# Kernel tuning notes

Hardware: AMD Instinct MI355X
Metric: run time of the kernel (lower is better)

Reference implementation:

```python
import jax, jax.numpy as jnp
import numpy as np


def mha(x, mask, wq, bq, wk, bk, wv, bv, wo, bo, n_heads):
    # Flaubert/XLM MultiHeadAttention (eval mode, dropout = identity).
    bs, qlen, dim = x.shape
    dph = dim // n_heads

    def split_heads(t):  # (bs, qlen, dim) -> (bs, n_heads, qlen, dph)
        return t.reshape(bs, qlen, n_heads, dph).transpose(0, 2, 1, 3)

    q = split_heads(x @ wq + bq) / jnp.sqrt(jnp.asarray(dph, x.dtype))
    k = split_heads(x @ wk + bk)
    v = split_heads(x @ wv + bv)

    scores = jnp.einsum('bhqd,bhkd->bhqk', q, k)  # (bs, h, qlen, klen)
    neg = jnp.finfo(scores.dtype).min
    scores = jnp.where((mask == 0)[:, None, None, :], neg, scores)
    weights = jax.nn.softmax(scores, axis=-1)
    ctx = jnp.einsum('bhqk,bhkd->bhqd', weights, v)
    ctx = ctx.transpose(0, 2, 1, 3).reshape(bs, qlen, dim)
    return ctx @ wo + bo


def setup_inputs() -> dict:
    key = jax.random.key(0)
    ks = jax.random.split(key, 20)
    bs, slen = 4, 1024
    d0, d1 = 192, 66
    std = 0.02
    inp = {
        'x': jax.random.normal(ks[0], (bs, slen, d0), jnp.float32),
        'y': jax.random.normal(ks[1], (bs, slen, d1), jnp.float32),
        'mask0': jax.random.randint(ks[2], (bs, slen), 0, 2, jnp.int32),
        'mask1': jax.random.randint(ks[3], (bs, slen), 0, 2, jnp.int32),
    }
    names0 = ['q0', 'k0', 'v0', 'o0']
    names1 = ['q1', 'k1', 'v1', 'o1']
    for i, n in enumerate(names0):
        inp[n + '_w'] = jax.random.normal(ks[4 + i], (d0, d0), jnp.float32) * std
        inp[n + '_b'] = jnp.zeros((d0,), jnp.float32)
    for i, n in enumerate(names1):
        inp[n + '_w'] = jax.random.normal(ks[8 + i], (d1, d1), jnp.float32) * std
        inp[n + '_b'] = jnp.zeros((d1,), jnp.float32)
    return inp


def reference(x, y, mask0, mask1,
              q0_w, q0_b, k0_w, k0_b, v0_w, v0_b, o0_w, o0_b,
              q1_w, q1_b, k1_w, k1_b, v1_w, v1_b, o1_w, o1_b):
    out0 = mha(x, mask0, q0_w, q0_b, k0_w, k0_b, v0_w, v0_b, o0_w, o0_b, n_heads=16)
    out1 = mha(y, mask1, q1_w, q1_b, k1_w, k1_b, v1_w, v1_b, o1_w, o1_b, n_heads=11)
    return (out0, out1)
```

## Files before the change

kernel.cpp:

```cpp
#include <hip/hip_runtime.h>
#include <math.h>


#define BS 4
#define SLEN 1024

#define Q0_OFF 0
#define C0_OFF 786432
#define Q1_OFF 1572864
#define C1_OFF 1843200
#define K0H_OFF 2113536
#define V0T_OFF 2506752
#define K1H_OFF 2899968
#define V1T_OFF 3080192
#define CNT_OFF 3223552

#define OUT0_SIZE 786432

#if __has_builtin(__builtin_amdgcn_exp2f)
#define EXP2(x) __builtin_amdgcn_exp2f(x)
#else
#define EXP2(x) __expf((x) * 0.69314718056f)
#endif

typedef _Float16 f16x2 __attribute__((ext_vector_type(2)));
typedef _Float16 f16x4 __attribute__((ext_vector_type(4)));
typedef _Float16 f16x8 __attribute__((ext_vector_type(8)));
typedef float f32x4 __attribute__((ext_vector_type(4)));

__device__ __forceinline__ void mfma_chunk(const _Float16* sA, const _Float16* sWT,
                                           int wv, int lane, f32x4 acc[4])
{
  const int col = lane & 15, grp = lane >> 4;
#pragma unroll
  for (int ks = 0; ks < 2; ++ks) {
    const f16x8 bf = *(const f16x8*)(sWT + (wv * 16 + col) * 72 + ks * 32 + grp * 8);
#pragma unroll
    for (int mt = 0; mt < 4; ++mt) {
      const f16x8 af = *(const f16x8*)(sA + (mt * 16 + col) * 72 + ks * 32 + grp * 8);
      acc[mt] = __builtin_amdgcn_mfma_f32_16x16x32_f16(af, bf, acc[mt], 0, 0, 0);
    }
  }
}

__device__ __forceinline__ void mfma_chunk_split(
    const _Float16* sAh, const _Float16* sAl,
    const _Float16* sWTh, const _Float16* sWTl,
    int wv, int lane, f32x4 acc[4])
{
  const int col = lane & 15, grp = lane >> 4;
#pragma unroll
  for (int ks = 0; ks < 2; ++ks) {
    const int boff = (wv * 16 + col) * 72 + ks * 32 + grp * 8;
    const f16x8 bh = *(const f16x8*)(sWTh + boff);
    const f16x8 bl = *(const f16x8*)(sWTl + boff);
#pragma unroll
    for (int mt = 0; mt < 4; ++mt) {
      const int aoff = (mt * 16 + col) * 72 + ks * 32 + grp * 8;
      const f16x8 ah = *(const f16x8*)(sAh + aoff);
      const f16x8 al = *(const f16x8*)(sAl + aoff);
      acc[mt] = __builtin_amdgcn_mfma_f32_16x16x32_f16(ah, bh, acc[mt], 0, 0, 0);
      acc[mt] = __builtin_amdgcn_mfma_f32_16x16x32_f16(ah, bl, acc[mt], 0, 0, 0);
      acc[mt] = __builtin_amdgcn_mfma_f32_16x16x32_f16(al, bh, acc[mt], 0, 0, 0);
    }
  }
}

template <int DIM, int H, int DPH, int NT, int NCH, int KST>
__device__ void qkv_impl(int bid, const float* __restrict__ X,
                         const int* __restrict__ mask,
                         const float* __restrict__ qw, const float* __restrict__ qb,
                         const float* __restrict__ kw, const float* __restrict__ kb,
                         const float* __restrict__ vw, const float* __restrict__ vb,
                         float* __restrict__ qo, _Float16* __restrict__ kh,
                         _Float16* __restrict__ vth, int* __restrict__ cnt_out,
                         char* smem)
{
  const int mt64 = bid & 63;
  const int rest = bid >> 6;
  const int mat = rest / NT;
  const int nt = rest % NT;
  const int row0 = mt64 * 64, col0 = nt * 64;

  const float* W = (mat == 0) ? qw : (mat == 1) ? kw : vw;
  const float* B = (mat == 0) ? qb : (mat == 1) ? kb : vb;
  const float scale = (mat == 0) ? (1.44269504089f / sqrtf((float)DPH)) : 1.0f;

  _Float16* sA = (_Float16*)smem;
  _Float16* sWT = sA + 64 * 72;
  int* sSP = (int*)(smem + 2 * 64 * 72 * 2);

  const int tid = threadIdx.x;
  const int wv = tid >> 6, lane = tid & 63;

  float2 rA[8], rW[8];
  auto qprefetch = [&](int c) {
    const int kc = c * 64;
#pragma unroll
    for (int t = 0; t < 8; ++t) {
      const int idx = tid + t * 256;
      {
        const int m = idx >> 5, k = (idx & 31) * 2;
        rA[t] = (kc + k < DIM)
                    ? *(const float2*)(X + (size_t)(row0 + m) * DIM + kc + k)
                    : make_float2(0.f, 0.f);
      }
      {
        const int k = idx >> 5, n = (idx & 31) * 2;
        rW[t] = (kc + k < DIM && col0 + n < DIM)
                    ? *(const float2*)(W + (size_t)(kc + k) * DIM + col0 + n)
                    : make_float2(0.f, 0.f);
      }
    }
  };
  auto qcommit = [&]() {
#pragma unroll
    for (int t = 0; t < 8; ++t) {
      const int idx = tid + t * 256;
      {
        const int m = idx >> 5, k = (idx & 31) * 2;
        *(f16x2*)(sA + m * 72 + k) = (f16x2){(_Float16)rA[t].x, (_Float16)rA[t].y};
      }
      {
        const int k = idx >> 5, n = (idx & 31) * 2;
        sWT[n * 72 + k] = (_Float16)rW[t].x;
        sWT[(n + 1) * 72 + k] = (_Float16)rW[t].y;
      }
    }
  };

  qprefetch(0);

  if (mat != 0) {
    int* sS = (int*)smem;
    const int b = row0 >> 10;
    const int* m = mask + (b << 10);
    int mv[4], s4 = 0;
#pragma unroll
    for (int i = 0; i < 4; ++i) { mv[i] = m[tid * 4 + i] ? 1 : 0; s4 += mv[i]; }
    sS[tid] = s4;
    __syncthreads();
    for (int off = 1; off < 256; off <<= 1) {
      const int v = sS[tid];
      const int add = (tid >= off) ? sS[tid - off] : 0;
      __syncthreads();
      sS[tid] = v + add;
      __syncthreads();
    }
    const int tot = sS[255];
    int u = tid ? sS[tid - 1] : 0;
    const int s0 = row0 & 1023;
#pragma unroll
    for (int i = 0; i < 4; ++i) {
      const int s = tid * 4 + i;
      const int sp = mv[i] ? u : tot + (s - u);
      u += mv[i];
      const unsigned rel = (unsigned)(s - s0);
      if (rel < 64u) sSP[rel] = sp;
    }
    if (mat == 1 && nt == 0 && s0 == 0 && tid == 0) cnt_out[b] = tot;
    __syncthreads();
  }

  f32x4 acc[4] = {{0.f,0.f,0.f,0.f},{0.f,0.f,0.f,0.f},{0.f,0.f,0.f,0.f},{0.f,0.f,0.f,0.f}};

  for (int c = 0; c < NCH; ++c) {
    __syncthreads();
    qcommit();
    __syncthreads();
    if (c + 1 < NCH) qprefetch(c + 1);
    mfma_chunk(sA, sWT, wv, lane, acc);
  }

  const int col = lane & 15, grp = lane >> 4;
  const int cidx = col0 + wv * 16 + col;
  if (cidx < DIM) {
    const float bias = B[cidx];
    const int h = cidx / DPH, d = cidx % DPH;
#pragma unroll
    for (int mt = 0; mt < 4; ++mt) {
#pragma unroll
      for (int r = 0; r < 4; ++r) {
        const int m = row0 + mt * 16 + grp * 4 + r;
        const int b = m >> 10, s = m & 1023;
        const float v = acc[mt][r] + bias;
        const int bh = b * H + h;
        if (mat == 0) {
          qo[(size_t)((bh << 10) + s) * DPH + d] = v * scale;
        } else {
          const int sp = sSP[mt * 16 + grp * 4 + r];
          if (mat == 1)
            kh[(size_t)((bh << 10) + sp) * KST + d] = (_Float16)v;
          else
            vth[((size_t)(bh * DPH + d) << 10) + sp] = (_Float16)v;
        }
      }
    }
  }
}

__global__ __launch_bounds__(256) void qkv_kernel(
    const float* __restrict__ x, const float* __restrict__ y,
    const int* __restrict__ mask0, const int* __restrict__ mask1,
    const float* __restrict__ q0w, const float* __restrict__ q0b,
    const float* __restrict__ k0w, const float* __restrict__ k0b,
    const float* __restrict__ v0w, const float* __restrict__ v0b,
    const float* __restrict__ q1w, const float* __restrict__ q1b,
    const float* __restrict__ k1w, const float* __restrict__ k1b,
    const float* __restrict__ v1w, const float* __restrict__ v1b,
    float* __restrict__ ws)
{
  extern __shared__ char smem[];
  _Float16* hws = (_Float16*)ws;
  int* cnts = (int*)(ws + CNT_OFF);
  const int bid = blockIdx.x;
  if (bid < 576)
    qkv_impl<192, 16, 12, 3, 3, 12>(bid, x, mask0, q0w, q0b, k0w, k0b, v0w, v0b,
                                    ws + Q0_OFF, hws + 2 * (size_t)K0H_OFF,
                                    hws + 2 * (size_t)V0T_OFF, cnts, smem);
  else
    qkv_impl<66, 11, 6, 2, 2, 8>(bid - 576, y, mask1, q1w, q1b, k1w, k1b, v1w, v1b,
                                 ws + Q1_OFF, hws + 2 * (size_t)K1H_OFF,
                                 hws + 2 * (size_t)V1T_OFF, cnts + 4, smem);
}

template <int H, int DPH, int SKP>
__device__ void attn_impl(int bid, const float* __restrict__ qg,
                          const _Float16* __restrict__ kh,
                          const _Float16* __restrict__ vth,
                          const int* __restrict__ cnts,
                          float* __restrict__ ctx, char* smem)
{
  constexpr int CH = 128;
  constexpr int KBUF = CH * SKP + 32;
  constexpr int VST = 136;

  _Float16* sK = (_Float16*)smem;
  _Float16* sVT = sK + 2 * KBUF;

  const int bh = bid >> 4;
  const int b = bh / H;
  const int h = bh % H;
  const int tid = threadIdx.x;

  const float* qb_ = qg + (size_t)bh * SLEN * DPH;
  const _Float16* kb_ = kh + (size_t)bh * SLEN * SKP;
  const _Float16* vb_ = vth + ((size_t)bh * DPH << 10);
  const int cnt = cnts[b];
  const int nch = (cnt + CH - 1) >> 7;

  if (tid < 64) sK[(tid >> 5) * KBUF + CH * SKP + (tid & 31)] = (_Float16)0.f;

  const int wave = tid >> 6, lane = tid & 63;
  const int col = lane & 15, grp = lane >> 4;
  const int qtile = (bid & 15) * 4 + wave;

  f16x4 aq;
  {
    const int qrow = qtile * 16 + col;
#pragma unroll
    for (int j = 0; j < 4; ++j) {
      const int d = grp * 4 + j;
      aq[j] = (d < DPH) ? (_Float16)qb_[(size_t)qrow * DPH + d] : (_Float16)0.f;
    }
  }

  constexpr int kN = CH * SKP / 8;
  constexpr int vN = DPH * 16;
  const int vd = tid >> 4, vq = tid & 15;
  uint4 pk, pv;
  auto prefetch = [&](int cc) {
    if (tid < kN) pk = ((const uint4*)(kb_ + (size_t)cc * CH * SKP))[tid];
    if (tid < vN) pv = ((const uint4*)(vb_ + ((size_t)vd << 10) + cc * CH))[vq];
  };
  auto commit = [&](int pb) {
    if (tid < kN) ((uint4*)(sK + pb * KBUF))[tid] = pk;
    if (tid < vN) *(uint4*)(sVT + (pb * DPH + vd) * VST + vq * 8) = pv;
  };

  prefetch(0);
  commit(0);
  __syncthreads();

  f32x4 Oacc[2] = {{0.f,0.f,0.f,0.f},{0.f,0.f,0.f,0.f}};
  float lsum = 0.f;
  const int de = (col < DPH) ? col : 0;

#pragma unroll 1
  for (int c = 0; c < nch; ++c) {
    const int p = c & 1;
    if (c + 1 < nch) prefetch(c + 1);

    const _Float16* sKp = sK + p * KBUF;
    const _Float16* sVp = sVT + p * DPH * VST;
    const int keyr = c * CH + grp * 4;

#pragma unroll
    for (int kt = 0; kt < CH / 16; ++kt) {
      const f16x4 kf = *(const f16x4*)(sKp + (kt * 16 + col) * SKP + grp * 4);
      const int k0 = keyr + kt * 16;
      const f32x4 biasv = {(k0 < cnt) ? 0.f : -100.f,
                           (k0 + 1 < cnt) ? 0.f : -100.f,
                           (k0 + 2 < cnt) ? 0.f : -100.f,
                           (k0 + 3 < cnt) ? 0.f : -100.f};
      const f32x4 S = __builtin_amdgcn_mfma_f32_16x16x16f16(kf, aq, biasv,
                                                            0, 0, 0);
      const float e0 = EXP2(S[0]), e1 = EXP2(S[1]);
      const float e2 = EXP2(S[2]), e3 = EXP2(S[3]);
      lsum += (e0 + e1) + (e2 + e3);
      const f16x4 pf = {(_Float16)e0, (_Float16)e1, (_Float16)e2, (_Float16)e3};
      const f16x4 vf = *(const f16x4*)(sVp + de * VST + kt * 16 + grp * 4);
      Oacc[kt & 1] = __builtin_amdgcn_mfma_f32_16x16x16f16(pf, vf, Oacc[kt & 1],
                                                           0, 0, 0);
    }

    if (c + 1 < nch) commit(p ^ 1);
    __syncthreads();
  }

  f32x4 Osum;
#pragma unroll
  for (int r = 0; r < 4; ++r) Osum[r] = Oacc[0][r] + Oacc[1][r];
  float lred = lsum;
  lred += __shfl_xor(lred, 16);
  lred += __shfl_xor(lred, 32);
  float lq[4];
#pragma unroll
  for (int r = 0; r < 4; ++r) lq[r] = __shfl(lred, grp * 4 + r);
  if (col < DPH) {
    const int qrow0 = qtile * 16;
#pragma unroll
    for (int r = 0; r < 4; ++r) {
      const int row = qrow0 + grp * 4 + r;
      ctx[(size_t)(b * SLEN + row) * (H * DPH) + h * DPH + col] = Osum[r] / lq[r];
    }
  }
}

__global__ __launch_bounds__(256) void attn_kernel(float* __restrict__ ws)
{
  extern __shared__ char smem[];
  _Float16* hws = (_Float16*)ws;
  const int* cnts = (const int*)(ws + CNT_OFF);
  const int G = gridDim.x;
#pragma unroll 1
  for (int it = blockIdx.x; it < 1728; it += G) {
    if (it < 1024)
      attn_impl<16, 12, 12>(it, ws + Q0_OFF, hws + 2 * (size_t)K0H_OFF,
                            hws + 2 * (size_t)V0T_OFF, cnts, ws + C0_OFF, smem);
    else
      attn_impl<11, 6, 8>(it - 1024, ws + Q1_OFF, hws + 2 * (size_t)K1H_OFF,
                          hws + 2 * (size_t)V1T_OFF, cnts + 4, ws + C1_OFF, smem);
  }
}

template <int DIM, int NCH>
__device__ void oproj_impl(int bid, const float* __restrict__ Cx,
                           const float* __restrict__ ow, const float* __restrict__ ob,
                           float* __restrict__ out, char* smem)
{
  const int mt64 = bid & 63;
  const int nt = bid >> 6;
  const int row0 = mt64 * 64, col0 = nt * 64;

  _Float16* sAh = (_Float16*)smem;
  _Float16* sAl = sAh + 64 * 72;
  _Float16* sWTh = sAl + 64 * 72;
  _Float16* sWTl = sWTh + 64 * 72;

  const int tid = threadIdx.x;
  const int wv = tid >> 6, lane = tid & 63;

  float2 rA[8], rW[8];
  auto oprefetch = [&](int c) {
    const int kc = c * 64;
#pragma unroll
    for (int t = 0; t < 8; ++t) {
      const int idx = tid + t * 256;
      {
        const int m = idx >> 5, k = (idx & 31) * 2;
        rA[t] = (kc + k < DIM)
                    ? *(const float2*)(Cx + (size_t)(row0 + m) * DIM + kc + k)
                    : make_float2(0.f, 0.f);
      }
      {
        const int k = idx >> 5, n = (idx & 31) * 2;
        rW[t] = (kc + k < DIM && col0 + n < DIM)
                    ? *(const float2*)(ow + (size_t)(kc + k) * DIM + col0 + n)
                    : make_float2(0.f, 0.f);
      }
    }
  };
  auto ocommit = [&]() {
#pragma unroll
    for (int t = 0; t < 8; ++t) {
      const int idx = tid + t * 256;
      {
        const int m = idx >> 5, k = (idx & 31) * 2;
        const _Float16 hx = (_Float16)rA[t].x, hy = (_Float16)rA[t].y;
        *(f16x2*)(sAh + m * 72 + k) = (f16x2){hx, hy};
        *(f16x2*)(sAl + m * 72 + k) =
            (f16x2){(_Float16)(rA[t].x - (float)hx), (_Float16)(rA[t].y - (float)hy)};
      }
      {
        const int k = idx >> 5, n = (idx & 31) * 2;
        const _Float16 hx = (_Float16)rW[t].x, hy = (_Float16)rW[t].y;
        sWTh[n * 72 + k] = hx;
        sWTh[(n + 1) * 72 + k] = hy;
        sWTl[n * 72 + k] = (_Float16)(rW[t].x - (float)hx);
        sWTl[(n + 1) * 72 + k] = (_Float16)(rW[t].y - (float)hy);
      }
    }
  };

  oprefetch(0);

  f32x4 acc[4] = {{0.f,0.f,0.f,0.f},{0.f,0.f,0.f,0.f},{0.f,0.f,0.f,0.f},{0.f,0.f,0.f,0.f}};

  for (int c = 0; c < NCH; ++c) {
    __syncthreads();
    ocommit();
    __syncthreads();
    if (c + 1 < NCH) oprefetch(c + 1);
    mfma_chunk_split(sAh, sAl, sWTh, sWTl, wv, lane, acc);
  }

  const int col = lane & 15, grp = lane >> 4;
  const int cidx = col0 + wv * 16 + col;
  if (cidx < DIM) {
    const float bias = ob[cidx];
#pragma unroll
    for (int mt = 0; mt < 4; ++mt) {
#pragma unroll
      for (int r = 0; r < 4; ++r) {
        const int m = row0 + mt * 16 + grp * 4 + r;
        out[(size_t)m * DIM + cidx] = acc[mt][r] + bias;
      }
    }
  }
}

__global__ __launch_bounds__(256) void oproj_kernel(
    const float* __restrict__ o0w, const float* __restrict__ o0b,
    const float* __restrict__ o1w, const float* __restrict__ o1b,
    float* __restrict__ ws, float* __restrict__ out)
{
  extern __shared__ char smem[];
  const int bid = blockIdx.x;
  if (bid < 192)
    oproj_impl<192, 3>(bid, ws + C0_OFF, o0w, o0b, out, smem);
  else
    oproj_impl<66, 2>(bid - 192, ws + C1_OFF, o1w, o1b, out + OUT0_SIZE, smem);
}

extern "C" void kernel_launch(void* const* d_in, const int* in_sizes, int n_in,
                              void* d_out, int out_size, void* d_ws, size_t ws_size,
                              hipStream_t stream)
{
  const float* x = (const float*)d_in[0];
  const float* y = (const float*)d_in[1];
  const int* mask0 = (const int*)d_in[2];
  const int* mask1 = (const int*)d_in[3];
  const float* q0w = (const float*)d_in[4];  const float* q0b = (const float*)d_in[5];
  const float* k0w = (const float*)d_in[6];  const float* k0b = (const float*)d_in[7];
  const float* v0w = (const float*)d_in[8];  const float* v0b = (const float*)d_in[9];
  const float* o0w = (const float*)d_in[10]; const float* o0b = (const float*)d_in[11];
  const float* q1w = (const float*)d_in[12]; const float* q1b = (const float*)d_in[13];
  const float* k1w = (const float*)d_in[14]; const float* k1b = (const float*)d_in[15];
  const float* v1w = (const float*)d_in[16]; const float* v1b = (const float*)d_in[17];
  const float* o1w = (const float*)d_in[18]; const float* o1b = (const float*)d_in[19];

  float* ws = (float*)d_ws;
  float* out = (float*)d_out;

  const int qkv_smem = 2 * 64 * 72 * 2 + 64 * 4;
  const int oproj_smem = 4 * 64 * 72 * 2;
  const int attn_smem = 2 * (128 * 12 + 32) * 2 + 2 * 12 * 136 * 2;

  qkv_kernel<<<960, 256, qkv_smem, stream>>>(x, y, mask0, mask1,
                                             q0w, q0b, k0w, k0b, v0w, v0b,
                                             q1w, q1b, k1w, k1b, v1w, v1b, ws);
  attn_kernel<<<1024, 256, attn_smem, stream>>>(ws);
  oproj_kernel<<<320, 256, oproj_smem, stream>>>(o0w, o0b, o1w, o1b, ws, out);
}
```

Baseline: 141.3 us.

## Double-buffer QKV shared tiles, pad LDS stride, use wave-shuffle mask scan

The QKV projection loop now double-buffers its shared-memory A and W tiles. The next chunk is committed into the alternate buffer after the MFMA work, so each iteration needs one barrier instead of two. The LDS row stride changes from 72 to 78 halves in both the QKV and output-projection GEMMs, meant to reduce bank conflicts. The mask prefix sum that was an LDS Hillis-Steele scan with many barriers becomes a wave-level shuffle scan plus a small cross-wave combine. The 78-half stride leaves 16-byte vector LDS reads misaligned, which may split or slow those accesses, and the double buffer doubles QKV shared-memory use.

```diff
diff --git a/kernel.cpp b/kernel.cpp
--- a/kernel.cpp
+++ b/kernel.cpp
@@ -17,6 +17,9 @@
 
 #define OUT0_SIZE 786432
 
+#define ST 78
+#define TILE (64 * ST)
+
 #if __has_builtin(__builtin_amdgcn_exp2f)
 #define EXP2(x) __builtin_amdgcn_exp2f(x)
 #else
@@ -34,10 +37,10 @@
   const int col = lane & 15, grp = lane >> 4;
 #pragma unroll
   for (int ks = 0; ks < 2; ++ks) {
-    const f16x8 bf = *(const f16x8*)(sWT + (wv * 16 + col) * 72 + ks * 32 + grp * 8);
+    const f16x8 bf = *(const f16x8*)(sWT + (wv * 16 + col) * ST + ks * 32 + grp * 8);
 #pragma unroll
     for (int mt = 0; mt < 4; ++mt) {
-      const f16x8 af = *(const f16x8*)(sA + (mt * 16 + col) * 72 + ks * 32 + grp * 8);
+      const f16x8 af = *(const f16x8*)(sA + (mt * 16 + col) * ST + ks * 32 + grp * 8);
       acc[mt] = __builtin_amdgcn_mfma_f32_16x16x32_f16(af, bf, acc[mt], 0, 0, 0);
     }
   }
@@ -51,12 +54,12 @@
   const int col = lane & 15, grp = lane >> 4;
 #pragma unroll
   for (int ks = 0; ks < 2; ++ks) {
-    const int boff = (wv * 16 + col) * 72 + ks * 32 + grp * 8;
+    const int boff = (wv * 16 + col) * ST + ks * 32 + grp * 8;
     const f16x8 bh = *(const f16x8*)(sWTh + boff);
     const f16x8 bl = *(const f16x8*)(sWTl + boff);
 #pragma unroll
     for (int mt = 0; mt < 4; ++mt) {
-      const int aoff = (mt * 16 + col) * 72 + ks * 32 + grp * 8;
+      const int aoff = (mt * 16 + col) * ST + ks * 32 + grp * 8;
       const f16x8 ah = *(const f16x8*)(sAh + aoff);
       const f16x8 al = *(const f16x8*)(sAl + aoff);
       acc[mt] = __builtin_amdgcn_mfma_f32_16x16x32_f16(ah, bh, acc[mt], 0, 0, 0);
@@ -87,8 +90,9 @@
   const float scale = (mat == 0) ? (1.44269504089f / sqrtf((float)DPH)) : 1.0f;
 
   _Float16* sA = (_Float16*)smem;
-  _Float16* sWT = sA + 64 * 72;
-  int* sSP = (int*)(smem + 2 * 64 * 72 * 2);
+  _Float16* sWT = sA + 2 * TILE;
+  int* sSP = (int*)(smem + 4 * TILE * 2);
+  int* sW4 = sSP + 64;
 
   const int tid = threadIdx.x;
   const int wv = tid >> 6, lane = tid & 63;
@@ -113,18 +117,20 @@
       }
     }
   };
-  auto qcommit = [&]() {
+  auto qcommit = [&](int pb) {
+    _Float16* dA = sA + pb * TILE;
+    _Float16* dW = sWT + pb * TILE;
 #pragma unroll
     for (int t = 0; t < 8; ++t) {
       const int idx = tid + t * 256;
       {
         const int m = idx >> 5, k = (idx & 31) * 2;
-        *(f16x2*)(sA + m * 72 + k) = (f16x2){(_Float16)rA[t].x, (_Float16)rA[t].y};
+        *(f16x2*)(dA + m * ST + k) = (f16x2){(_Float16)rA[t].x, (_Float16)rA[t].y};
       }
       {
         const int k = idx >> 5, n = (idx & 31) * 2;
-        sWT[n * 72 + k] = (_Float16)rW[t].x;
-        sWT[(n + 1) * 72 + k] = (_Float16)rW[t].y;
+        dW[n * ST + k] = (_Float16)rW[t].x;
+        dW[(n + 1) * ST + k] = (_Float16)rW[t].y;
       }
     }
   };
@@ -132,23 +138,27 @@
   qprefetch(0);
 
   if (mat != 0) {
-    int* sS = (int*)smem;
     const int b = row0 >> 10;
     const int* m = mask + (b << 10);
     int mv[4], s4 = 0;
 #pragma unroll
     for (int i = 0; i < 4; ++i) { mv[i] = m[tid * 4 + i] ? 1 : 0; s4 += mv[i]; }
-    sS[tid] = s4;
-    __syncthreads();
-    for (int off = 1; off < 256; off <<= 1) {
-      const int v = sS[tid];
-      const int add = (tid >= off) ? sS[tid - off] : 0;
-      __syncthreads();
-      sS[tid] = v + add;
-      __syncthreads();
-    }
-    const int tot = sS[255];
-    int u = tid ? sS[tid - 1] : 0;
+    int ps = s4;
+#pragma unroll
+    for (int off = 1; off < 64; off <<= 1) {
+      const int v = __shfl_up(ps, off);
+      if (lane >= off) ps += v;
+    }
+    if (lane == 63) sW4[wv] = ps;
+    __syncthreads();
+    int wbase = 0, tot = 0;
+#pragma unroll
+    for (int w = 0; w < 4; ++w) {
+      const int t = sW4[w];
+      tot += t;
+      if (w < wv) wbase += t;
+    }
+    int u = wbase + ps - s4;
     const int s0 = row0 & 1023;
 #pragma unroll
     for (int i = 0; i < 4; ++i) {
@@ -164,12 +174,15 @@
 
   f32x4 acc[4] = {{0.f,0.f,0.f,0.f},{0.f,0.f,0.f,0.f},{0.f,0.f,0.f,0.f},{0.f,0.f,0.f,0.f}};
 
+  qcommit(0);
+  __syncthreads();
+#pragma unroll 1
   for (int c = 0; c < NCH; ++c) {
-    __syncthreads();
-    qcommit();
-    __syncthreads();
+    const int p = c & 1;
     if (c + 1 < NCH) qprefetch(c + 1);
-    mfma_chunk(sA, sWT, wv, lane, acc);
+    mfma_chunk(sA + p * TILE, sWT + p * TILE, wv, lane, acc);
+    if (c + 1 < NCH) qcommit(p ^ 1);
+    __syncthreads();
   }
 
   const int col = lane & 15, grp = lane >> 4;
@@ -364,9 +377,9 @@
   const int row0 = mt64 * 64, col0 = nt * 64;
 
   _Float16* sAh = (_Float16*)smem;
-  _Float16* sAl = sAh + 64 * 72;
-  _Float16* sWTh = sAl + 64 * 72;
-  _Float16* sWTl = sWTh + 64 * 72;
+  _Float16* sAl = sAh + TILE;
+  _Float16* sWTh = sAl + TILE;
+  _Float16* sWTl = sWTh + TILE;
 
   const int tid = threadIdx.x;
   const int wv = tid >> 6, lane = tid & 63;
@@ -398,17 +411,17 @@
       {
         const int m = idx >> 5, k = (idx & 31) * 2;
         const _Float16 hx = (_Float16)rA[t].x, hy = (_Float16)rA[t].y;
-        *(f16x2*)(sAh + m * 72 + k) = (f16x2){hx, hy};
-        *(f16x2*)(sAl + m * 72 + k) =
+        *(f16x2*)(sAh + m * ST + k) = (f16x2){hx, hy};
+        *(f16x2*)(sAl + m * ST + k) =
             (f16x2){(_Float16)(rA[t].x - (float)hx), (_Float16)(rA[t].y - (float)hy)};
       }
       {
         const int k = idx >> 5, n = (idx & 31) * 2;
         const _Float16 hx = (_Float16)rW[t].x, hy = (_Float16)rW[t].y;
-        sWTh[n * 72 + k] = hx;
-        sWTh[(n + 1) * 72 + k] = hy;
-        sWTl[n * 72 + k] = (_Float16)(rW[t].x - (float)hx);
-        sWTl[(n + 1) * 72 + k] = (_Float16)(rW[t].y - (float)hy);
+        sWTh[n * ST + k] = hx;
+        sWTh[(n + 1) * ST + k] = hy;
+        sWTl[n * ST + k] = (_Float16)(rW[t].x - (float)hx);
+        sWTl[(n + 1) * ST + k] = (_Float16)(rW[t].y - (float)hy);
       }
     }
   };
@@ -473,8 +486,8 @@
   float* ws = (float*)d_ws;
   float* out = (float*)d_out;
 
-  const int qkv_smem = 2 * 64 * 72 * 2 + 64 * 4;
-  const int oproj_smem = 4 * 64 * 72 * 2;
+  const int qkv_smem = 4 * TILE * 2 + 68 * 4;
+  const int oproj_smem = 4 * TILE * 2;
   const int attn_smem = 2 * (128 * 12 + 32) * 2 + 2 * 12 * 136 * 2;
 
   qkv_kernel<<<960, 256, qkv_smem, stream>>>(x, y, mask0, mask1,
```

New measurement: 153.9 us. 1.09x slower.

## Coalesce QKV epilogue stores: row-major Q, skip padded K/V, LDS-transposed V

Applied to the files above, without the earlier changes.

Q is now written in row-major (token, dim) layout instead of head-split, and the attention kernel indexes it with stride DIM. K and V stores skip compacted positions beyond the 128-rounded count of valid keys, since attention never reads those chunks. V is transposed through shared memory so each thread writes along the sequence dimension, which gives more contiguous stores into the transposed V buffer. The cost is extra barriers and LDS traffic in the V path.

```diff
diff --git a/kernel.cpp b/kernel.cpp
--- a/kernel.cpp
+++ b/kernel.cpp
@@ -131,6 +131,7 @@
 
   qprefetch(0);
 
+  int totKV = 0;
   if (mat != 0) {
     int* sS = (int*)smem;
     const int b = row0 >> 10;
@@ -148,6 +149,7 @@
       __syncthreads();
     }
     const int tot = sS[255];
+    totKV = tot;
     int u = tid ? sS[tid - 1] : 0;
     const int s0 = row0 & 1023;
 #pragma unroll
@@ -174,25 +176,59 @@
 
   const int col = lane & 15, grp = lane >> 4;
   const int cidx = col0 + wv * 16 + col;
-  if (cidx < DIM) {
-    const float bias = B[cidx];
-    const int h = cidx / DPH, d = cidx % DPH;
-#pragma unroll
-    for (int mt = 0; mt < 4; ++mt) {
-#pragma unroll
-      for (int r = 0; r < 4; ++r) {
-        const int m = row0 + mt * 16 + grp * 4 + r;
-        const int b = m >> 10, s = m & 1023;
-        const float v = acc[mt][r] + bias;
-        const int bh = b * H + h;
-        if (mat == 0) {
-          qo[(size_t)((bh << 10) + s) * DPH + d] = v * scale;
-        } else {
+  const int slim = ((totKV + 127) >> 7) << 7;
+
+  if (mat == 0) {
+    if (cidx < DIM) {
+      const float bias = B[cidx];
+#pragma unroll
+      for (int mt = 0; mt < 4; ++mt)
+#pragma unroll
+        for (int r = 0; r < 4; ++r) {
+          const int m = row0 + mt * 16 + grp * 4 + r;
+          qo[(size_t)m * DIM + cidx] = (acc[mt][r] + bias) * scale;
+        }
+    }
+  } else if (mat == 1) {
+    if (cidx < DIM) {
+      const float bias = B[cidx];
+      const int h = cidx / DPH, d = cidx % DPH;
+#pragma unroll
+      for (int mt = 0; mt < 4; ++mt)
+#pragma unroll
+        for (int r = 0; r < 4; ++r) {
+          const int m = row0 + mt * 16 + grp * 4 + r;
+          const int b = m >> 10;
           const int sp = sSP[mt * 16 + grp * 4 + r];
-          if (mat == 1)
-            kh[(size_t)((bh << 10) + sp) * KST + d] = (_Float16)v;
-          else
-            vth[((size_t)(bh * DPH + d) << 10) + sp] = (_Float16)v;
+          if (sp < slim)
+            kh[(size_t)(((b * H + h) << 10) + sp) * KST + d] =
+                (_Float16)(acc[mt][r] + bias);
+        }
+    }
+  } else {
+    _Float16* sT = (_Float16*)smem;
+    __syncthreads();
+    if (cidx < DIM) {
+      const float bias = B[cidx];
+      const int colI = wv * 16 + col;
+#pragma unroll
+      for (int mt = 0; mt < 4; ++mt)
+#pragma unroll
+        for (int r = 0; r < 4; ++r)
+          sT[colI * 68 + mt * 16 + grp * 4 + r] = (_Float16)(acc[mt][r] + bias);
+    }
+    __syncthreads();
+    const int sl = tid & 63, cq = tid >> 6;
+    const int b = row0 >> 10;
+    const int sp = sSP[sl];
+    if (sp < slim) {
+#pragma unroll
+      for (int p = 0; p < 16; ++p) {
+        const int colI = p * 4 + cq;
+        const int c2 = col0 + colI;
+        if (c2 < DIM) {
+          const int h = c2 / DPH, d = c2 % DPH;
+          vth[((size_t)((b * H + h) * DPH + d) << 10) + sp] = sT[colI * 68 + sl];
         }
       }
     }
@@ -234,6 +270,7 @@
   constexpr int CH = 128;
   constexpr int KBUF = CH * SKP + 32;
   constexpr int VST = 136;
+  constexpr int DIMQ = H * DPH;
 
   _Float16* sK = (_Float16*)smem;
   _Float16* sVT = sK + 2 * KBUF;
@@ -243,7 +280,7 @@
   const int h = bh % H;
   const int tid = threadIdx.x;
 
-  const float* qb_ = qg + (size_t)bh * SLEN * DPH;
+  const float* qb_ = qg + ((size_t)b << 10) * DIMQ + h * DPH;
   const _Float16* kb_ = kh + (size_t)bh * SLEN * SKP;
   const _Float16* vb_ = vth + ((size_t)bh * DPH << 10);
   const int cnt = cnts[b];
@@ -261,7 +298,7 @@
 #pragma unroll
     for (int j = 0; j < 4; ++j) {
       const int d = grp * 4 + j;
-      aq[j] = (d < DPH) ? (_Float16)qb_[(size_t)qrow * DPH + d] : (_Float16)0.f;
+      aq[j] = (d < DPH) ? (_Float16)qb_[(size_t)qrow * DIMQ + d] : (_Float16)0.f;
     }
   }
 
```

New measurement: 143.0 us. About the same (+1.2%).
